# Kernel optimization log

Measured on AMD Instinct MI355X. Metric: run time of the kernel, lower is better.

The kernel has to match this reference:

```python
import jax, jax.numpy as jnp
import numpy as np

B, S, T = 64, 1024, 64
H, A, DA, DT, P, NT = 1024, 1024, 512, 256, 256, 32
DIN = DA + A + DT  # LSTMCell input: [a_tm1_embed, att_tm1, pre_type]


def setup_inputs() -> dict:
    key = jax.random.key(0)
    ks = jax.random.split(key, 16)
    nrm = lambda k, shape, s=0.02: jax.random.normal(k, shape, jnp.float32) * s
    return {
        'src_encodings': jax.random.normal(ks[0], (B, S, H), jnp.float32),
        'W_ih': nrm(ks[1], (4 * H, DIN)), 'b_ih': jnp.zeros((4 * H,), jnp.float32),
        'W_hh': nrm(ks[2], (4 * H, H)), 'b_hh': jnp.zeros((4 * H,), jnp.float32),
        'W_att': nrm(ks[3], (H, H)),            # att_sketch_linear (no bias)
        'W_attvec': nrm(ks[4], (A, 2 * H)),     # sketch_att_vec_linear (no bias)
        'W_init': nrm(ks[5], (H, H)), 'b_init': jnp.zeros((H,), jnp.float32),  # decoder_cell_init
        'W_q2a': nrm(ks[6], (DA, A)), 'b_q2a': jnp.zeros((DA,), jnp.float32),  # query_vec_to_action_embed
        'prod_embed': nrm(ks[7], (P, DA), 0.05), 'prod_bias': jnp.zeros((P,), jnp.float32),
        'type_embed': nrm(ks[8], (NT, DT), 0.05),
        'prev_prod_ids': jax.random.randint(ks[9], (B, T), 0, P),
        'prev_type_ids': jax.random.randint(ks[10], (B, T), 0, NT),
        'target_prod_ids': jax.random.randint(ks[11], (B, T), 0, P),
        'sketch_lens': jax.random.randint(ks[12], (B,), T // 2, T + 1),
        'src_lens': jax.random.randint(ks[13], (B,), S // 2, S + 1),
    }


def _lstm_cell(x, h, c, W_ih, b_ih, W_hh, b_hh):
    gates = x @ W_ih.T + b_ih + h @ W_hh.T + b_hh
    i, f, g, o = jnp.split(gates, 4, axis=-1)
    c_new = jax.nn.sigmoid(f) * c + jax.nn.sigmoid(i) * jnp.tanh(g)
    h_new = jax.nn.sigmoid(o) * jnp.tanh(c_new)
    return h_new, c_new


def reference(src_encodings, W_ih, b_ih, W_hh, b_hh, W_att, W_attvec, W_init, b_init,
              W_q2a, b_q2a, prod_embed, prod_bias, type_embed,
              prev_prod_ids, prev_type_ids, target_prod_ids, sketch_lens, src_lens):
    Bq, Sq, Hq = src_encodings.shape
    Tq = prev_prod_ids.shape[1]
    src_valid = jnp.arange(Sq)[None, :] < src_lens[:, None]            # [B,S] True = real token
    step_valid = jnp.arange(Tq)[None, :] < sketch_lens[:, None]        # [B,T]
    prev_valid = step_valid & (jnp.arange(Tq)[None, :] > 0)            # prev action exists

    src_att = jnp.einsum('bsh,kh->bsk', src_encodings, W_att)          # att_sketch_linear
    # init_decoder_state(adaptive_avg_pool1d(enc,1))
    init_cell = src_encodings.mean(axis=1)
    h0 = jnp.tanh(init_cell @ W_init.T + b_init)
    c0 = jnp.zeros_like(h0)
    att0 = jnp.zeros((Bq, A), src_encodings.dtype)

    # precomputed grammar lookups (production / type embeddings of a_{t-1})
    a_embeds = jnp.where(prev_valid[..., None], prod_embed[prev_prod_ids], 0.0)   # [B,T,DA]
    t_embeds = jnp.where(prev_valid[..., None], type_embed[prev_type_ids], 0.0)   # [B,T,DT]
    is_first = jnp.arange(Tq) == 0                                                # [T]

    def step(carry, inp):
        h, c, att_tm1 = carry
        a_e, t_e, first = inp
        x = jnp.concatenate([a_e, att_tm1, t_e], axis=-1)
        x = jnp.where(first, 0.0, x)                                   # t==0 -> zero input
        h, c = _lstm_cell(x, h, c, W_ih, b_ih, W_hh, b_hh)
        scores = jnp.einsum('bh,bsh->bs', h, src_att)
        scores = jnp.where(src_valid, scores, -1e9)
        alpha = jax.nn.softmax(scores, axis=-1)
        ctx = jnp.einsum('bs,bsh->bh', alpha, src_encodings)
        att_t = jnp.tanh(jnp.concatenate([h, ctx], axis=-1) @ W_attvec.T)
        q = jnp.tanh(att_t @ W_q2a.T + b_q2a)                          # non_linear readout
        probs = jax.nn.softmax(q @ prod_embed.T + prod_bias, axis=-1)  # [B,P]
        return (h, c, att_t), probs

    xs = (jnp.swapaxes(a_embeds, 0, 1), jnp.swapaxes(t_embeds, 0, 1), is_first)
    _, probs = jax.lax.scan(step, (h0, c0, att0), xs)                  # [T,B,P]

    tgt = jnp.swapaxes(target_prod_ids, 0, 1)[..., None]               # [T,B,1]
    p_t = jnp.take_along_axis(probs, tgt, axis=-1)[..., 0]             # [T,B]
    logp = jnp.log(p_t + 1e-8)
    sketch_prob = jnp.sum(jnp.where(step_valid.T, logp, 0.0), axis=0)  # [B]
    return sketch_prob
```

## Files before the change

kernel.cpp:

```cpp
#include <hip/hip_runtime.h>
#include <hip/hip_bf16.h>

typedef unsigned short u16;
typedef unsigned int u32;
typedef unsigned long long u64;
typedef __attribute__((ext_vector_type(8))) short short8;
typedef __attribute__((ext_vector_type(8))) u16 ushort8;
typedef __attribute__((ext_vector_type(4))) float f32x4;

__device__ __forceinline__ float bf2f(u16 x){ u32 u=((u32)x)<<16; return __builtin_bit_cast(float,u); }
__device__ __forceinline__ u16 f2bf(float f){ u32 u=__builtin_bit_cast(u32,f); u32 r=(u+0x7fffu+((u>>16)&1u))>>16; return (u16)r; }
__device__ __forceinline__ float sigf(float x){ return 1.f/(1.f+__expf(-x)); }

__device__ __forceinline__ void scf(float* p, float v){
  __hip_atomic_store(p, v, __ATOMIC_RELAXED, __HIP_MEMORY_SCOPE_AGENT);
}
__device__ __forceinline__ void scu16(u16* p, u16 v){
  __hip_atomic_store(p, v, __ATOMIC_RELAXED, __HIP_MEMORY_SCOPE_AGENT);
}


__global__ __launch_bounds__(256) void k_cast(const float* __restrict__ s, u16* __restrict__ d, long n){
  long i = ((long)blockIdx.x*256 + threadIdx.x)*8;
  if (i >= n) return;
  float4 a = *(const float4*)(s+i);
  float4 b = *(const float4*)(s+i+4);
  ushort8 o;
  o[0]=f2bf(a.x); o[1]=f2bf(a.y); o[2]=f2bf(a.z); o[3]=f2bf(a.w);
  o[4]=f2bf(b.x); o[5]=f2bf(b.y); o[6]=f2bf(b.z); o[7]=f2bf(b.w);
  *(ushort8*)(d+i) = o;
}

__global__ __launch_bounds__(256) void k_build_wc(const float* __restrict__ Wih, const float* __restrict__ Whh,
                                                  u16* __restrict__ WC){
  long i8 = (long)blockIdx.x*256 + threadIdx.x;
  if (i8 >= (long)4096*352) return;
  int j = (int)(i8/352); int kk = (int)(i8%352)*8;
  const float* src;
  if (kk < 512)        src = Wih + (long)j*1792 + kk;
  else if (kk < 768)   src = Wih + (long)j*1792 + (kk+1024);
  else if (kk < 1792)  src = Wih + (long)j*1792 + (kk-256);
  else                 src = Whh + (long)j*1024 + (kk-1792);
  u16* dst = WC + (long)j*2816 + kk;
  ushort8 o;
  #pragma unroll
  for (int q=0;q<8;++q) o[q] = f2bf(src[q]);
  *(ushort8*)dst = o;
}

__global__ __launch_bounds__(256) void k_wattT(const float* __restrict__ Wa, u16* __restrict__ WT){
  int id = blockIdx.x*256 + threadIdx.x;
  int m = id >> 10, k = id & 1023;
  WT[(long)m*1024 + k] = f2bf(Wa[(long)k*1024 + m]);
}

__global__ __launch_bounds__(256) void k_mean(const u16* __restrict__ ENC, u16* __restrict__ MEANB){
  int b = blockIdx.x, h = blockIdx.y*256 + threadIdx.x;
  const u16* p = ENC + ((long)b<<20) + h;
  float s = 0.f;
  for (int ss=0; ss<1024; ++ss) s += bf2f(p[(long)ss<<10]);
  MEANB[b*1024 + h] = f2bf(s * (1.f/1024.f));
}

__global__ __launch_bounds__(256) void k_embed(const float* __restrict__ pemb, const float* __restrict__ temb,
      const int* __restrict__ pid, const int* __restrict__ tid_, const int* __restrict__ slen,
      u16* __restrict__ XC){
  int t = blockIdx.x >> 6, b = blockIdx.x & 63;
  bool valid = (t>0) && (t < slen[b]);
  int pi = pid[b*64 + t], ti = tid_[b*64 + t];
  u16* dst = XC + (long)blockIdx.x*2816;
  for (int kk = threadIdx.x; kk < 768; kk += 256){
    float v = 0.f;
    if (valid) v = (kk<512) ? pemb[(long)pi*512 + kk] : temb[(long)ti*256 + (kk-512)];
    dst[kk] = f2bf(v);
  }
}

__global__ void k_assign(const int* __restrict__ slen, int* __restrict__ ASG){
  if (threadIdx.x != 0 || blockIdx.x != 0) return;
  int lenv[64]; long total = 0;
  for (int b=0;b<64;++b){ int L = slen[b]; if (L<1)L=1; if (L>1024)L=1024; lenv[b]=L; total+=L; }
  int cnt[64]; int sum=0;
  for (int b=0;b<64;++b){ int c = (int)(((long)256*lenv[b])/total); if (c<1)c=1; cnt[b]=c; sum+=c; }
  int rem = 256 - sum; int bi = 0;
  while (rem > 0){ cnt[bi&63]++; rem--; bi++; }
  while (rem < 0){ if (cnt[bi&63] > 1){ cnt[bi&63]--; rem++; } bi++; }
  int st = 0;
  for (int b=0;b<64;++b){
    ASG[1024+b] = cnt[b];
    ASG[1088+b] = st;
    for (int i=0;i<cnt[b];++i){ ASG[st+i] = b; ASG[256+st+i] = i; }
    st += cnt[b];
  }
}

template<int MODE>
__global__ __launch_bounds__(256) void k_gemm(const u16* __restrict__ A, long lda,
      const u16* __restrict__ W, int K, const float* __restrict__ bias,
      float* __restrict__ OF, long ldo, u16* __restrict__ OB1, long ldb1){
  int l = threadIdx.x & 63, w = threadIdx.x >> 6;
  int c = l & 15, g = l >> 4;
  int n0 = blockIdx.x*16, m0 = blockIdx.y*64;
  const u16* ap = A + (long)(m0 + w*16 + c)*lda + g*8;
  const u16* bp = W + (long)(n0 + c)*K + g*8;
  f32x4 acc = {0.f,0.f,0.f,0.f};
  int kit = K >> 5;
  #pragma unroll 4
  for (int kb=0; kb<kit; ++kb){
    short8 av = *(const short8*)(ap + kb*32);
    short8 bv = *(const short8*)(bp + kb*32);
    acc = __builtin_amdgcn_mfma_f32_16x16x32_bf16(av, bv, acc, 0, 0, 0);
  }
  #pragma unroll
  for (int r=0;r<4;++r){
    int row = m0 + w*16 + g*4 + r;
    int col = n0 + c;
    float v = acc[r];
    if (MODE==2){ OB1[(long)row*ldb1 + col] = f2bf(tanhf(v + bias[col])); }
    if (MODE==3){ OF[(long)row*ldo + col] = v + bias[col]; }
  }
}

__global__ __launch_bounds__(256) void k_loss(const float* __restrict__ LG, const int* __restrict__ tgt,
      const int* __restrict__ slen, float* __restrict__ out){
  int b = blockIdx.x;
  int w = threadIdx.x >> 6, l = threadIdx.x & 63;
  int len = slen[b];
  float accum = 0.f;
  for (int t = w; t < 64; t += 4){
    if (t >= len) continue;
    const float* lp = LG + ((long)(t*64 + b))*256;
    float v0=lp[l], v1=lp[l+64], v2=lp[l+128], v3=lp[l+192];
    float mx = fmaxf(fmaxf(v0,v1), fmaxf(v2,v3));
    #pragma unroll
    for (int off=32; off; off>>=1) mx = fmaxf(mx, __shfl_xor(mx, off));
    float s = __expf(v0-mx)+__expf(v1-mx)+__expf(v2-mx)+__expf(v3-mx);
    #pragma unroll
    for (int off=32; off; off>>=1) s += __shfl_xor(s, off);
    float ltg = lp[tgt[b*64 + t]];
    float p = __expf(ltg - mx)/s;
    accum += logf(p + 1e-8f);
  }
  __shared__ float sm[4];
  if (l == 0) sm[w] = accum;
  __syncthreads();
  if (threadIdx.x == 0) out[b] = sm[0]+sm[1]+sm[2]+sm[3];
}

__device__ __forceinline__ void gsync(int* __restrict__ bar, int& gen){
  gen += 1;
  __syncthreads();
  if (threadIdx.x == 0){
    int grp = blockIdx.x & 15;
    int prev = __hip_atomic_fetch_add(bar + grp*64, 1, __ATOMIC_RELAXED, __HIP_MEMORY_SCOPE_AGENT);
    if (prev == gen*16 - 1)
      __hip_atomic_fetch_add(bar + 1024, 1, __ATOMIC_RELAXED, __HIP_MEMORY_SCOPE_AGENT);
    while (__hip_atomic_load(bar + 1024, __ATOMIC_RELAXED, __HIP_MEMORY_SCOPE_AGENT) < gen*16)
      __builtin_amdgcn_s_sleep(1);
  }
  __syncthreads();
}

__global__ __launch_bounds__(1024,1) void k_decoder(
      const u16* __restrict__ ENC, const u16* __restrict__ WC,
      const u16* __restrict__ WAVT, const u16* __restrict__ WAVEC,
      const float* __restrict__ bih, const float* __restrict__ bhh,
      u16* __restrict__ XC, u16* __restrict__ ATT,
      float* __restrict__ HWT, float* __restrict__ PLT,
      u16* __restrict__ CTXBT, const int* __restrict__ src_lens,
      const int* __restrict__ ASG, int* __restrict__ BAR){
  const int tid = threadIdx.x;
  const int w = tid >> 6, l = tid & 63, c = l & 15, g = l >> 4;
  const int bx = blockIdx.x;
  int gen = 0;

  __shared__ float smem[12320];
  f32x4* lacc  = (f32x4*)smem;
  float* s_ctx = smem;
  float* s_ls  = smem + 12288;
  u16*   ldsc  = (u16*)smem;
  f32x4* lacc4 = (f32x4*)(smem + 8192);

  const int n0 = bx << 2;
  const int jrow = n0 + (c & 3) + ((c >> 2) << 10);
  const float biasj = bih[jrow] + bhh[jrow];
  const int kh = w >> 2, mt = w & 3;
  const int lbase = l & 0x33;
  float creg[4] = {0.f,0.f,0.f,0.f};
  const int mt2 = bx & 3, nt2 = bx >> 2;
  const int b3 = ASG[bx];
  const int ci3 = ASG[256 + bx];
  const int nch3 = ASG[1024 + b3];
  int len3 = src_lens[b3]; if (len3 < 1) len3 = 1; if (len3 > 1024) len3 = 1024;
  const int chunk3 = (len3 + nch3 - 1)/nch3;
  int s0 = ci3*chunk3;
  int s1 = s0 + chunk3; if (s1 > len3) s1 = len3; if (s0 > s1) s0 = s1;
  const int mt4 = bx & 3, nt4 = bx >> 2;
  const int b16 = tid >> 6, lane64 = tid & 63;

  for (int t = 0; t < 64; ++t){
    const u16* XCt = XC + (size_t)t*64*2816;
    u16* XCn = XC + (size_t)(t+1)*64*2816;
    const u16* Hcur = XCn + 1792;
    float* HW   = HWT  + ((size_t)t<<16);
    float* PL   = PLT  + ((size_t)t<<8);
    u16*  CTXB  = CTXBT + ((size_t)t<<18);

    {
      const u16* ap = XCt + (long)(mt*16 + c)*2816 + kh*704 + g*8;
      const u16* bp = WC  + (long)jrow*2816 + kh*704 + g*8;
      f32x4 acc = {0.f,0.f,0.f,0.f};
      #pragma unroll 11
      for (int kb=0; kb<22; ++kb){
        short8 av = *(const short8*)(ap + kb*32);
        short8 bv = *(const short8*)(bp + kb*32);
        acc = __builtin_amdgcn_mfma_f32_16x16x32_bf16(av, bv, acc, 0, 0, 0);
      }
      lacc[w*64 + l] = acc;
      __syncthreads();
      if (w < 4){
        f32x4 a0 = lacc[w*64 + l];
        f32x4 a1 = lacc[(w+4)*64 + l];
        f32x4 a2 = lacc[(w+8)*64 + l];
        f32x4 a3 = lacc[(w+12)*64 + l];
        #pragma unroll
        for (int r=0;r<4;++r){
          float val = a0[r] + a1[r] + a2[r] + a3[r] + biasj;
          float iv = __shfl(val, lbase);
          float fv = __shfl(val, lbase+4);
          float gv = __shfl(val, lbase+8);
          float ov = __shfl(val, lbase+12);
          if ((l & 12) == 0){
            float cn = sigf(fv)*creg[r] + sigf(iv)*tanhf(gv);
            float hn = sigf(ov)*tanhf(cn);
            creg[r] = cn;
            int b = w*16 + g*4 + r;
            int n = n0 + (l & 3);
            scu16(XCn + (long)b*2816 + 1792 + n, f2bf(hn));
          }
        }
      }
    }
    gsync(BAR, gen);

    {
      const u16* ap = Hcur + (long)(mt2*16 + c)*2816 + w*64 + g*8;
      const u16* bp = WAVT + (long)(nt2*16 + c)*1024 + w*64 + g*8;
      f32x4 acc = {0.f,0.f,0.f,0.f};
      #pragma unroll
      for (int kb=0; kb<2; ++kb){
        short8 av = *(const short8*)(ap + kb*32);
        short8 bv = *(const short8*)(bp + kb*32);
        acc = __builtin_amdgcn_mfma_f32_16x16x32_bf16(av, bv, acc, 0, 0, 0);
      }
      lacc[w*64 + l] = acc;
      __syncthreads();
      if (w == 0){
        f32x4 rd = lacc[l];
        #pragma unroll
        for (int w2=1; w2<16; ++w2) rd += lacc[w2*64 + l];
        #pragma unroll
        for (int r=0;r<4;++r)
          scf(HW + (long)(mt2*16 + g*4 + r)*1024 + nt2*16 + c, rd[r]);
      }
    }
    gsync(BAR, gen);

    {
      float hw[16], ctx[16];
      const float* hwp = HW + b3*1024 + l*16;
      #pragma unroll
      for (int jj=0;jj<4;++jj){
        float4 v = *(const float4*)(hwp + jj*4);
        hw[4*jj]=v.x; hw[4*jj+1]=v.y; hw[4*jj+2]=v.z; hw[4*jj+3]=v.w;
      }
      #pragma unroll
      for (int jj=0;jj<16;++jj) ctx[jj]=0.f;
      float lsum = 0.f;
      const u16* encb = ENC + (((long)b3)<<20);
      const int base = s0 + 2*w;
      uint4 pa0,pa1,pa2,pa3, pb0,pb1,pb2,pb3, pc0,pc1,pc2,pc3;
      {
        int rA0 = (base   < s1) ? base   : s0;
        int rA1 = (base+1 < s1) ? base+1 : s0;
        const u16* p0 = encb + ((long)rA0<<10) + l*16;
        const u16* p1 = encb + ((long)rA1<<10) + l*16;
        pa0=*(const uint4*)p0; pa1=*(const uint4*)(p0+8);
        pa2=*(const uint4*)p1; pa3=*(const uint4*)(p1+8);
        int sB = base+32;
        int rB0 = (sB   < s1) ? sB   : s0;
        int rB1 = (sB+1 < s1) ? sB+1 : s0;
        const u16* q0 = encb + ((long)rB0<<10) + l*16;
        const u16* q1 = encb + ((long)rB1<<10) + l*16;
        pb0=*(const uint4*)q0; pb1=*(const uint4*)(q0+8);
        pb2=*(const uint4*)q1; pb3=*(const uint4*)(q1+8);
      }
      for (int s = base; s < s1; s += 32){
        int sC = s + 64;
        int rC0 = (sC   < s1) ? sC   : s0;
        int rC1 = (sC+1 < s1) ? sC+1 : s0;
        const u16* r0p = encb + ((long)rC0<<10) + l*16;
        const u16* r1p = encb + ((long)rC1<<10) + l*16;
        pc0=*(const uint4*)r0p; pc1=*(const uint4*)(r0p+8);
        pc2=*(const uint4*)r1p; pc3=*(const uint4*)(r1p+8);
        float scA = 0.f, scB = 0.f;
        #pragma unroll
        for (int jj=0;jj<4;++jj){
          u32 xA0=((const u32*)&pa0)[jj], xA1=((const u32*)&pa1)[jj];
          u32 xB0=((const u32*)&pa2)[jj], xB1=((const u32*)&pa3)[jj];
          scA += bf2f((u16)(xA0&0xffff))*hw[2*jj]   + bf2f((u16)(xA0>>16))*hw[2*jj+1];
          scA += bf2f((u16)(xA1&0xffff))*hw[8+2*jj] + bf2f((u16)(xA1>>16))*hw[8+2*jj+1];
          scB += bf2f((u16)(xB0&0xffff))*hw[2*jj]   + bf2f((u16)(xB0>>16))*hw[2*jj+1];
          scB += bf2f((u16)(xB1&0xffff))*hw[8+2*jj] + bf2f((u16)(xB1>>16))*hw[8+2*jj+1];
        }
        #pragma unroll
        for (int off=32; off; off>>=1){
          scA += __shfl_xor(scA, off);
          scB += __shfl_xor(scB, off);
        }
        if (s+1 >= s1) scB = -1e30f;
        float peA = __expf(scA);
        float peB = __expf(scB);
        lsum += peA + peB;
        #pragma unroll
        for (int jj=0;jj<4;++jj){
          u32 xA0=((const u32*)&pa0)[jj], xA1=((const u32*)&pa1)[jj];
          u32 xB0=((const u32*)&pa2)[jj], xB1=((const u32*)&pa3)[jj];
          ctx[2*jj]     += peA*bf2f((u16)(xA0&0xffff)) + peB*bf2f((u16)(xB0&0xffff));
          ctx[2*jj+1]   += peA*bf2f((u16)(xA0>>16))    + peB*bf2f((u16)(xB0>>16));
          ctx[8+2*jj]   += peA*bf2f((u16)(xA1&0xffff)) + peB*bf2f((u16)(xB1&0xffff));
          ctx[8+2*jj+1] += peA*bf2f((u16)(xA1>>16))    + peB*bf2f((u16)(xB1>>16));
        }
        pa0=pb0; pa1=pb1; pa2=pb2; pa3=pb3;
        pb0=pc0; pb1=pc1; pb2=pc2; pb3=pc3;
      }
      if (l == 0) s_ls[w] = lsum;
      if (w < 8){
        #pragma unroll
        for (int jj=0;jj<16;++jj) s_ctx[w*1024 + l*16 + jj] = ctx[jj];
      }
      __syncthreads();
      if (w >= 8){
        #pragma unroll
        for (int jj=0;jj<16;++jj) s_ctx[(w-8)*1024 + l*16 + jj] += ctx[jj];
      }
      __syncthreads();
      {
        float v = 0.f;
        #pragma unroll
        for (int p=0;p<8;++p) v += s_ctx[p*1024 + tid];
        scu16(CTXB + (((long)bx)<<10) + tid, f2bf(v));
      }
      if (tid == 0){
        float L = 0.f;
        #pragma unroll
        for (int q=0;q<16;++q) L += s_ls[q];
        scf(PL + bx, L);
      }
    }
    gsync(BAR, gen);

    {
      int b = mt4*16 + b16;
      int st = ASG[1088 + b], nL = ASG[1024 + b];
      float L = 0.f;
      for (int p=0;p<nL;++p) L += PL[st+p];
      float inv = (L > 0.f) ? 1.f/L : 0.f;
      float acc16[16];
      #pragma unroll
      for (int q=0;q<16;++q) acc16[q] = 0.f;
      for (int p=0;p<nL;++p){
        const u16* row = CTXB + (((long)(st+p))<<10);
        #pragma unroll
        for (int q=0;q<2;++q){
          int mcol8 = (lane64 + q*64)*8;
          ushort8 v = *(const ushort8*)(row + mcol8);
          #pragma unroll
          for (int j=0;j<8;++j) acc16[q*8+j] += bf2f(v[j]);
        }
      }
      const int swz = (b16 & 7) << 3;
      #pragma unroll
      for (int q=0;q<2;++q){
        int mcol8 = (lane64 + q*64)*8;
        ushort8 o;
        #pragma unroll
        for (int j=0;j<8;++j) o[j] = f2bf(acc16[q*8+j]*inv);
        *(ushort8*)(ldsc + ((b16*1024 + mcol8) ^ swz)) = o;
      }
      __syncthreads();
      f32x4 acc = {0.f,0.f,0.f,0.f};
      const int koff = (w < 8) ? w*128 : 1024 + (w-8)*128;
      const u16* bp = WAVEC + (long)(nt4*16 + c)*2048 + koff + g*8;
      if (w < 8){
        const u16* ap = Hcur + (long)(mt4*16 + c)*2816 + w*128 + g*8;
        #pragma unroll
        for (int kb=0; kb<4; ++kb){
          short8 av = *(const short8*)(ap + kb*32);
          short8 bv = *(const short8*)(bp + kb*32);
          acc = __builtin_amdgcn_mfma_f32_16x16x32_bf16(av, bv, acc, 0, 0, 0);
        }
      } else {
        const int cswz = (c & 7) << 3;
        const int kbase = c*1024 + (w-8)*128 + g*8;
        #pragma unroll
        for (int kb=0; kb<4; ++kb){
          short8 av = *(const short8*)(ldsc + ((kbase + kb*32) ^ cswz));
          short8 bv = *(const short8*)(bp + kb*32);
          acc = __builtin_amdgcn_mfma_f32_16x16x32_bf16(av, bv, acc, 0, 0, 0);
        }
      }
      lacc4[w*64 + l] = acc;
      __syncthreads();
      if (w == 0){
        f32x4 rd = lacc4[l];
        #pragma unroll
        for (int w2=1; w2<16; ++w2) rd += lacc4[w2*64 + l];
        #pragma unroll
        for (int r=0;r<4;++r){
          int b_ = mt4*16 + g*4 + r;
          int col = nt4*16 + c;
          u16 x = f2bf(tanhf(rd[r]));
          scu16(XCn + (long)b_*2816 + 768 + col, x);
          ATT[((long)t*64 + b_)*1024 + col] = x;
        }
      }
    }
    gsync(BAR, gen);
  }
}

extern "C" void kernel_launch(void* const* d_in, const int* in_sizes, int n_in,
                              void* d_out, int out_size, void* d_ws, size_t ws_size,
                              hipStream_t stream){
  const float* enc      = (const float*)d_in[0];
  const float* W_ih     = (const float*)d_in[1];
  const float* b_ih     = (const float*)d_in[2];
  const float* W_hh     = (const float*)d_in[3];
  const float* b_hh     = (const float*)d_in[4];
  const float* W_att    = (const float*)d_in[5];
  const float* W_attvec = (const float*)d_in[6];
  const float* W_init   = (const float*)d_in[7];
  const float* b_init   = (const float*)d_in[8];
  const float* W_q2a    = (const float*)d_in[9];
  const float* b_q2a    = (const float*)d_in[10];
  const float* prod_emb = (const float*)d_in[11];
  const float* prod_bias= (const float*)d_in[12];
  const float* type_emb = (const float*)d_in[13];
  const int* prev_pid   = (const int*)d_in[14];
  const int* prev_tid   = (const int*)d_in[15];
  const int* target     = (const int*)d_in[16];
  const int* sk_lens    = (const int*)d_in[17];
  const int* src_lens   = (const int*)d_in[18];
  float* out = (float*)d_out;

  char* ws = (char*)d_ws;
  size_t o = 0;
  auto alloc = [&](size_t bytes)->char*{ char* p = ws + o; o += (bytes + 255) & ~(size_t)255; return p; };
  u16*  ENC  = (u16*)alloc((size_t)64*1024*1024*2);
  u16*  WC   = (u16*)alloc((size_t)4096*2816*2);
  u16*  WAVT = (u16*)alloc((size_t)1024*1024*2);
  u16*  WAVEC= (u16*)alloc((size_t)1024*2048*2);
  u16*  WQ   = (u16*)alloc((size_t)512*1024*2);
  u16*  PE   = (u16*)alloc((size_t)256*512*2);
  u16*  WINIT= (u16*)alloc((size_t)1024*1024*2);
  u16*  MEANB= (u16*)alloc((size_t)64*1024*2);
  u16*  XC   = (u16*)alloc((size_t)65*64*2816*2);
  u16*  ATT  = (u16*)alloc((size_t)64*64*1024*2);
  float* HWT = (float*)alloc((size_t)64*64*1024*4);
  float* PLT = (float*)alloc((size_t)64*256*4);
  u16*  CTXBT=(u16*)alloc((size_t)64*256*1024*2);
  u16*  Q    = (u16*)alloc((size_t)4096*512*2);
  float* LG  = (float*)alloc((size_t)4096*256*4);
  int*  BAR  = (int*)alloc(8192);
  int*  ASG  = (int*)alloc(8192);
  (void)ws_size; (void)in_sizes; (void)n_in; (void)out_size;

  hipMemsetAsync(XC, 0, (size_t)64*2816*2, stream);
  hipMemsetAsync(BAR, 0, 8192, stream);

  k_assign<<<1,64,0,stream>>>(src_lens, ASG);
  k_cast<<<32768,256,0,stream>>>(enc, ENC, (long)64*1024*1024);
  k_cast<<<1024,256,0,stream>>>(W_attvec, WAVEC, (long)1024*2048);
  k_cast<<<256,256,0,stream>>>(W_q2a, WQ, (long)512*1024);
  k_cast<<<64,256,0,stream>>>(prod_emb, PE, (long)256*512);
  k_cast<<<512,256,0,stream>>>(W_init, WINIT, (long)1024*1024);
  k_build_wc<<<5632,256,0,stream>>>(W_ih, W_hh, WC);
  k_wattT<<<4096,256,0,stream>>>(W_att, WAVT);
  k_mean<<<dim3(64,4),256,0,stream>>>(ENC, MEANB);
  k_gemm<2><<<dim3(64,1),256,0,stream>>>(MEANB, 1024L, WINIT, 1024, b_init,
                                         nullptr, 0L, XC + 1792, 2816L);
  k_embed<<<4096,256,0,stream>>>(prod_emb, type_emb, prev_pid, prev_tid, sk_lens, XC);

  k_decoder<<<256,1024,0,stream>>>(ENC, WC, WAVT, WAVEC, b_ih, b_hh,
                                   XC, ATT, HWT, PLT, CTXBT, src_lens, ASG, BAR);

  k_gemm<2><<<dim3(32,64),256,0,stream>>>(ATT, 1024L, WQ, 1024, b_q2a,
                                          nullptr, 0L, Q, 512L);
  k_gemm<3><<<dim3(16,64),256,0,stream>>>(Q, 512L, PE, 512, prod_bias,
                                          LG, 256L, nullptr, 0L);
  k_loss<<<64,256,0,stream>>>(LG, target, sk_lens, out);
}
```

Before: 4.395 ms.

## Precompute embedding gate contribution, relax barrier, prefetch encodings across steps

Moves the input-to-gate product for the action and type embeddings out of the recurrent loop into one batched GEMM before the decoder, so each step's LSTM matmul only covers attention and hidden inputs (K drops from 2816 to 2048). It replaces one global barrier with per-batch-group done counters, so blocks wait only for the context chunks their group needs. It also caps each batch at 8 chunks, which lets the chunk-sum reads be unrolled. Encoding rows are prefetched before the step loop and the reloads are moved after the attention loop, so the next step's loads overlap other work. The trade-offs are a 32MB buffer of precomputed gate values read every step and more complex synchronization.

```diff
diff --git a/kernel.cpp b/kernel.cpp
--- a/kernel.cpp
+++ b/kernel.cpp
@@ -64,11 +64,11 @@
 
 __global__ __launch_bounds__(256) void k_embed(const float* __restrict__ pemb, const float* __restrict__ temb,
       const int* __restrict__ pid, const int* __restrict__ tid_, const int* __restrict__ slen,
-      u16* __restrict__ XC){
+      u16* __restrict__ EMB){
   int t = blockIdx.x >> 6, b = blockIdx.x & 63;
   bool valid = (t>0) && (t < slen[b]);
   int pi = pid[b*64 + t], ti = tid_[b*64 + t];
-  u16* dst = XC + (long)blockIdx.x*2816;
+  u16* dst = EMB + (long)blockIdx.x*768;
   for (int kk = threadIdx.x; kk < 768; kk += 256){
     float v = 0.f;
     if (valid) v = (kk<512) ? pemb[(long)pi*512 + kk] : temb[(long)ti*256 + (kk-512)];
@@ -81,9 +81,12 @@
   int lenv[64]; long total = 0;
   for (int b=0;b<64;++b){ int L = slen[b]; if (L<1)L=1; if (L>1024)L=1024; lenv[b]=L; total+=L; }
   int cnt[64]; int sum=0;
-  for (int b=0;b<64;++b){ int c = (int)(((long)256*lenv[b])/total); if (c<1)c=1; cnt[b]=c; sum+=c; }
+  for (int b=0;b<64;++b){
+    int c = (int)(((long)256*lenv[b])/total);
+    if (c<1)c=1; if (c>8)c=8; cnt[b]=c; sum+=c;
+  }
   int rem = 256 - sum; int bi = 0;
-  while (rem > 0){ cnt[bi&63]++; rem--; bi++; }
+  while (rem > 0){ if (cnt[bi&63] < 8){ cnt[bi&63]++; rem--; } bi++; }
   while (rem < 0){ if (cnt[bi&63] > 1){ cnt[bi&63]--; rem++; } bi++; }
   int st = 0;
   for (int b=0;b<64;++b){
@@ -92,17 +95,22 @@
     for (int i=0;i<cnt[b];++i){ ASG[st+i] = b; ASG[256+st+i] = i; }
     st += cnt[b];
   }
+  for (int g=0; g<4; ++g){
+    int tg = 0;
+    for (int i=0;i<16;++i) tg += cnt[g*16+i];
+    ASG[1156+g] = tg;
+  }
 }
 
 template<int MODE>
 __global__ __launch_bounds__(256) void k_gemm(const u16* __restrict__ A, long lda,
-      const u16* __restrict__ W, int K, const float* __restrict__ bias,
+      const u16* __restrict__ W, long wld, int K, const float* __restrict__ bias,
       float* __restrict__ OF, long ldo, u16* __restrict__ OB1, long ldb1){
   int l = threadIdx.x & 63, w = threadIdx.x >> 6;
   int c = l & 15, g = l >> 4;
   int n0 = blockIdx.x*16, m0 = blockIdx.y*64;
   const u16* ap = A + (long)(m0 + w*16 + c)*lda + g*8;
-  const u16* bp = W + (long)(n0 + c)*K + g*8;
+  const u16* bp = W + (long)(n0 + c)*wld + g*8;
   f32x4 acc = {0.f,0.f,0.f,0.f};
   int kit = K >> 5;
   #pragma unroll 4
@@ -118,6 +126,7 @@
     float v = acc[r];
     if (MODE==2){ OB1[(long)row*ldb1 + col] = f2bf(tanhf(v + bias[col])); }
     if (MODE==3){ OF[(long)row*ldo + col] = v + bias[col]; }
+    if (MODE==4){ OB1[(long)row*ldb1 + col] = f2bf(v); }
   }
 }
 
@@ -164,11 +173,12 @@
 __global__ __launch_bounds__(1024,1) void k_decoder(
       const u16* __restrict__ ENC, const u16* __restrict__ WC,
       const u16* __restrict__ WAVT, const u16* __restrict__ WAVEC,
+      const u16* __restrict__ GEMB,
       const float* __restrict__ bih, const float* __restrict__ bhh,
       u16* __restrict__ XC, u16* __restrict__ ATT,
       float* __restrict__ HWT, float* __restrict__ PLT,
       u16* __restrict__ CTXBT, const int* __restrict__ src_lens,
-      const int* __restrict__ ASG, int* __restrict__ BAR){
+      const int* __restrict__ ASG, int* __restrict__ BAR, int* __restrict__ DONE){
   const int tid = threadIdx.x;
   const int w = tid >> 6, l = tid & 63, c = l & 15, g = l >> 4;
   const int bx = blockIdx.x;
@@ -191,27 +201,56 @@
   const int b3 = ASG[bx];
   const int ci3 = ASG[256 + bx];
   const int nch3 = ASG[1024 + b3];
+  const int g3 = b3 >> 4;
   int len3 = src_lens[b3]; if (len3 < 1) len3 = 1; if (len3 > 1024) len3 = 1024;
   const int chunk3 = (len3 + nch3 - 1)/nch3;
   int s0 = ci3*chunk3;
   int s1 = s0 + chunk3; if (s1 > len3) s1 = len3; if (s0 > s1) s0 = s1;
+  const u16* encb = ENC + (((long)b3)<<20);
+  const int base = s0 + 2*w;
   const int mt4 = bx & 3, nt4 = bx >> 2;
   const int b16 = tid >> 6, lane64 = tid & 63;
+  const int tgt4 = ASG[1156 + mt4];
+
+  uint4 pa0,pa1,pa2,pa3, pb0,pb1,pb2,pb3;
+  {
+    int rA0 = (base   < s1) ? base   : s0;
+    int rA1 = (base+1 < s1) ? base+1 : s0;
+    const u16* p0 = encb + ((long)rA0<<10) + l*16;
+    const u16* p1 = encb + ((long)rA1<<10) + l*16;
+    pa0=*(const uint4*)p0; pa1=*(const uint4*)(p0+8);
+    pa2=*(const uint4*)p1; pa3=*(const uint4*)(p1+8);
+    int sB = base+32;
+    int rB0 = (sB   < s1) ? sB   : s0;
+    int rB1 = (sB+1 < s1) ? sB+1 : s0;
+    const u16* q0 = encb + ((long)rB0<<10) + l*16;
+    const u16* q1 = encb + ((long)rB1<<10) + l*16;
+    pb0=*(const uint4*)q0; pb1=*(const uint4*)(q0+8);
+    pb2=*(const uint4*)q1; pb3=*(const uint4*)(q1+8);
+  }
 
   for (int t = 0; t < 64; ++t){
-    const u16* XCt = XC + (size_t)t*64*2816;
-    u16* XCn = XC + (size_t)(t+1)*64*2816;
-    const u16* Hcur = XCn + 1792;
+    const u16* XCt = XC + (size_t)t*64*2048;
+    u16* XCn = XC + (size_t)(t+1)*64*2048;
+    const u16* Hcur = XCn + 1024;
     float* HW   = HWT  + ((size_t)t<<16);
     float* PL   = PLT  + ((size_t)t<<8);
     u16*  CTXB  = CTXBT + ((size_t)t<<18);
 
     {
-      const u16* ap = XCt + (long)(mt*16 + c)*2816 + kh*704 + g*8;
-      const u16* bp = WC  + (long)jrow*2816 + kh*704 + g*8;
+      float gb[4];
+      if (w < 4){
+        #pragma unroll
+        for (int r=0;r<4;++r){
+          int b = w*16 + g*4 + r;
+          gb[r] = bf2f(GEMB[(((size_t)t*64 + b))*4096 + jrow]);
+        }
+      }
+      const u16* ap = XCt + (long)(mt*16 + c)*2048 + kh*512 + g*8;
+      const u16* bp = WC  + (long)jrow*2816 + 768 + kh*512 + g*8;
       f32x4 acc = {0.f,0.f,0.f,0.f};
-      #pragma unroll 11
-      for (int kb=0; kb<22; ++kb){
+      #pragma unroll 8
+      for (int kb=0; kb<16; ++kb){
         short8 av = *(const short8*)(ap + kb*32);
         short8 bv = *(const short8*)(bp + kb*32);
         acc = __builtin_amdgcn_mfma_f32_16x16x32_bf16(av, bv, acc, 0, 0, 0);
@@ -225,7 +264,7 @@
         f32x4 a3 = lacc[(w+12)*64 + l];
         #pragma unroll
         for (int r=0;r<4;++r){
-          float val = a0[r] + a1[r] + a2[r] + a3[r] + biasj;
+          float val = a0[r] + a1[r] + a2[r] + a3[r] + gb[r] + biasj;
           float iv = __shfl(val, lbase);
           float fv = __shfl(val, lbase+4);
           float gv = __shfl(val, lbase+8);
@@ -236,7 +275,7 @@
             creg[r] = cn;
             int b = w*16 + g*4 + r;
             int n = n0 + (l & 3);
-            scu16(XCn + (long)b*2816 + 1792 + n, f2bf(hn));
+            scu16(XCn + (long)b*2048 + 1024 + n, f2bf(hn));
           }
         }
       }
@@ -244,7 +283,7 @@
     gsync(BAR, gen);
 
     {
-      const u16* ap = Hcur + (long)(mt2*16 + c)*2816 + w*64 + g*8;
+      const u16* ap = Hcur + (long)(mt2*16 + c)*2048 + w*64 + g*8;
       const u16* bp = WAVT + (long)(nt2*16 + c)*1024 + w*64 + g*8;
       f32x4 acc = {0.f,0.f,0.f,0.f};
       #pragma unroll
@@ -277,9 +316,45 @@
       #pragma unroll
       for (int jj=0;jj<16;++jj) ctx[jj]=0.f;
       float lsum = 0.f;
-      const u16* encb = ENC + (((long)b3)<<20);
-      const int base = s0 + 2*w;
-      uint4 pa0,pa1,pa2,pa3, pb0,pb1,pb2,pb3, pc0,pc1,pc2,pc3;
+      for (int s = base; s < s1; s += 32){
+        int sC = s + 64;
+        int rC0 = (sC   < s1) ? sC   : s0;
+        int rC1 = (sC+1 < s1) ? sC+1 : s0;
+        const u16* r0p = encb + ((long)rC0<<10) + l*16;
+        const u16* r1p = encb + ((long)rC1<<10) + l*16;
+        uint4 pc0=*(const uint4*)r0p; uint4 pc1=*(const uint4*)(r0p+8);
+        uint4 pc2=*(const uint4*)r1p; uint4 pc3=*(const uint4*)(r1p+8);
+        float scA = 0.f, scB = 0.f;
+        #pragma unroll
+        for (int jj=0;jj<4;++jj){
+          u32 xA0=((const u32*)&pa0)[jj], xA1=((const u32*)&pa1)[jj];
+          u32 xB0=((const u32*)&pa2)[jj], xB1=((const u32*)&pa3)[jj];
+          scA += bf2f((u16)(xA0&0xffff))*hw[2*jj]   + bf2f((u16)(xA0>>16))*hw[2*jj+1];
+          scA += bf2f((u16)(xA1&0xffff))*hw[8+2*jj] + bf2f((u16)(xA1>>16))*hw[8+2*jj+1];
+          scB += bf2f((u16)(xB0&0xffff))*hw[2*jj]   + bf2f((u16)(xB0>>16))*hw[2*jj+1];
+          scB += bf2f((u16)(xB1&0xffff))*hw[8+2*jj] + bf2f((u16)(xB1>>16))*hw[8+2*jj+1];
+        }
+        #pragma unroll
+        for (int off=32; off; off>>=1){
+          scA += __shfl_xor(scA, off);
+          scB += __shfl_xor(scB, off);
+        }
+        if (s+1 >= s1) scB = -1e30f;
+        float peA = __expf(scA);
+        float peB = __expf(scB);
+        lsum += peA + peB;
+        #pragma unroll
+        for (int jj=0;jj<4;++jj){
+          u32 xA0=((const u32*)&pa0)[jj], xA1=((const u32*)&pa1)[jj];
+          u32 xB0=((const u32*)&pa2)[jj], xB1=((const u32*)&pa3)[jj];
+          ctx[2*jj]     += peA*bf2f((u16)(xA0&0xffff)) + peB*bf2f((u16)(xB0&0xffff));
+          ctx[2*jj+1]   += peA*bf2f((u16)(xA0>>16))    + peB*bf2f((u16)(xB0>>16));
+          ctx[8+2*jj]   += peA*bf2f((u16)(xA1&0xffff)) + peB*bf2f((u16)(xB1&0xffff));
+          ctx[8+2*jj+1] += peA*bf2f((u16)(xA1>>16))    + peB*bf2f((u16)(xB1>>16));
+        }
+        pa0=pb0; pa1=pb1; pa2=pb2; pa3=pb3;
+        pb0=pc0; pb1=pc1; pb2=pc2; pb3=pc3;
+      }
       {
         int rA0 = (base   < s1) ? base   : s0;
         int rA1 = (base+1 < s1) ? base+1 : s0;
@@ -295,45 +370,6 @@
         pb0=*(const uint4*)q0; pb1=*(const uint4*)(q0+8);
         pb2=*(const uint4*)q1; pb3=*(const uint4*)(q1+8);
       }
-      for (int s = base; s < s1; s += 32){
-        int sC = s + 64;
-        int rC0 = (sC   < s1) ? sC   : s0;
-        int rC1 = (sC+1 < s1) ? sC+1 : s0;
-        const u16* r0p = encb + ((long)rC0<<10) + l*16;
-        const u16* r1p = encb + ((long)rC1<<10) + l*16;
-        pc0=*(const uint4*)r0p; pc1=*(const uint4*)(r0p+8);
-        pc2=*(const uint4*)r1p; pc3=*(const uint4*)(r1p+8);
-        float scA = 0.f, scB = 0.f;
-        #pragma unroll
-        for (int jj=0;jj<4;++jj){
-          u32 xA0=((const u32*)&pa0)[jj], xA1=((const u32*)&pa1)[jj];
-          u32 xB0=((const u32*)&pa2)[jj], xB1=((const u32*)&pa3)[jj];
-          scA += bf2f((u16)(xA0&0xffff))*hw[2*jj]   + bf2f((u16)(xA0>>16))*hw[2*jj+1];
-          scA += bf2f((u16)(xA1&0xffff))*hw[8+2*jj] + bf2f((u16)(xA1>>16))*hw[8+2*jj+1];
-          scB += bf2f((u16)(xB0&0xffff))*hw[2*jj]   + bf2f((u16)(xB0>>16))*hw[2*jj+1];
-          scB += bf2f((u16)(xB1&0xffff))*hw[8+2*jj] + bf2f((u16)(xB1>>16))*hw[8+2*jj+1];
-        }
-        #pragma unroll
-        for (int off=32; off; off>>=1){
-          scA += __shfl_xor(scA, off);
-          scB += __shfl_xor(scB, off);
-        }
-        if (s+1 >= s1) scB = -1e30f;
-        float peA = __expf(scA);
-        float peB = __expf(scB);
-        lsum += peA + peB;
-        #pragma unroll
-        for (int jj=0;jj<4;++jj){
-          u32 xA0=((const u32*)&pa0)[jj], xA1=((const u32*)&pa1)[jj];
-          u32 xB0=((const u32*)&pa2)[jj], xB1=((const u32*)&pa3)[jj];
-          ctx[2*jj]     += peA*bf2f((u16)(xA0&0xffff)) + peB*bf2f((u16)(xB0&0xffff));
-          ctx[2*jj+1]   += peA*bf2f((u16)(xA0>>16))    + peB*bf2f((u16)(xB0>>16));
-          ctx[8+2*jj]   += peA*bf2f((u16)(xA1&0xffff)) + peB*bf2f((u16)(xB1&0xffff));
-          ctx[8+2*jj+1] += peA*bf2f((u16)(xA1>>16))    + peB*bf2f((u16)(xB1>>16));
-        }
-        pa0=pb0; pa1=pb1; pa2=pb2; pa3=pb3;
-        pb0=pc0; pb1=pc1; pb2=pc2; pb3=pc3;
-      }
       if (l == 0) s_ls[w] = lsum;
       if (w < 8){
         #pragma unroll
@@ -358,25 +394,47 @@
         scf(PL + bx, L);
       }
     }
-    gsync(BAR, gen);
+    __syncthreads();
+    if (tid == 0){
+      __hip_atomic_fetch_add(DONE + t*4 + g3, 1, __ATOMIC_RELAXED, __HIP_MEMORY_SCOPE_AGENT);
+      while (__hip_atomic_load(DONE + t*4 + mt4, __ATOMIC_RELAXED, __HIP_MEMORY_SCOPE_AGENT) < tgt4)
+        __builtin_amdgcn_s_sleep(1);
+    }
+    __syncthreads();
 
     {
       int b = mt4*16 + b16;
       int st = ASG[1088 + b], nL = ASG[1024 + b];
+      float plv[8];
+      #pragma unroll
+      for (int p=0;p<8;++p){ int ip = st + ((p<nL)? p:0); plv[p] = PL[ip]; }
       float L = 0.f;
-      for (int p=0;p<nL;++p) L += PL[st+p];
+      #pragma unroll
+      for (int p=0;p<8;++p) if (p<nL) L += plv[p];
       float inv = (L > 0.f) ? 1.f/L : 0.f;
       float acc16[16];
       #pragma unroll
       for (int q=0;q<16;++q) acc16[q] = 0.f;
-      for (int p=0;p<nL;++p){
-        const u16* row = CTXB + (((long)(st+p))<<10);
-        #pragma unroll
-        for (int q=0;q<2;++q){
-          int mcol8 = (lane64 + q*64)*8;
-          ushort8 v = *(const ushort8*)(row + mcol8);
-          #pragma unroll
-          for (int j=0;j<8;++j) acc16[q*8+j] += bf2f(v[j]);
+      #pragma unroll
+      for (int rnd=0; rnd<2; ++rnd){
+        ushort8 va[4][2];
+        #pragma unroll
+        for (int q4=0;q4<4;++q4){
+          int p = rnd*4+q4; int ip = st + ((p<nL)? p:0);
+          const u16* row = CTXB + (((long)ip)<<10);
+          va[q4][0] = *(const ushort8*)(row + lane64*8);
+          va[q4][1] = *(const ushort8*)(row + (lane64+64)*8);
+        }
+        #pragma unroll
+        for (int q4=0;q4<4;++q4){
+          int p = rnd*4+q4;
+          if (p<nL){
+            #pragma unroll
+            for (int j=0;j<8;++j){
+              acc16[j]   += bf2f(va[q4][0][j]);
+              acc16[8+j] += bf2f(va[q4][1][j]);
+            }
+          }
         }
       }
       const int swz = (b16 & 7) << 3;
@@ -393,7 +451,7 @@
       const int koff = (w < 8) ? w*128 : 1024 + (w-8)*128;
       const u16* bp = WAVEC + (long)(nt4*16 + c)*2048 + koff + g*8;
       if (w < 8){
-        const u16* ap = Hcur + (long)(mt4*16 + c)*2816 + w*128 + g*8;
+        const u16* ap = Hcur + (long)(mt4*16 + c)*2048 + w*128 + g*8;
         #pragma unroll
         for (int kb=0; kb<4; ++kb){
           short8 av = *(const short8*)(ap + kb*32);
@@ -421,7 +479,7 @@
           int b_ = mt4*16 + g*4 + r;
           int col = nt4*16 + c;
           u16 x = f2bf(tanhf(rd[r]));
-          scu16(XCn + (long)b_*2816 + 768 + col, x);
+          scu16(XCn + (long)b_*2048 + col, x);
           ATT[((long)t*64 + b_)*1024 + col] = x;
         }
       }
@@ -465,7 +523,9 @@
   u16*  PE   = (u16*)alloc((size_t)256*512*2);
   u16*  WINIT= (u16*)alloc((size_t)1024*1024*2);
   u16*  MEANB= (u16*)alloc((size_t)64*1024*2);
-  u16*  XC   = (u16*)alloc((size_t)65*64*2816*2);
+  u16*  EMB  = (u16*)alloc((size_t)4096*768*2);
+  u16*  GEMB = (u16*)alloc((size_t)4096*4096*2);
+  u16*  XC   = (u16*)alloc((size_t)65*64*2048*2);
   u16*  ATT  = (u16*)alloc((size_t)64*64*1024*2);
   float* HWT = (float*)alloc((size_t)64*64*1024*4);
   float* PLT = (float*)alloc((size_t)64*256*4);
@@ -473,11 +533,13 @@
   u16*  Q    = (u16*)alloc((size_t)4096*512*2);
   float* LG  = (float*)alloc((size_t)4096*256*4);
   int*  BAR  = (int*)alloc(8192);
+  int*  DONE = (int*)alloc(4096);
   int*  ASG  = (int*)alloc(8192);
   (void)ws_size; (void)in_sizes; (void)n_in; (void)out_size;
 
-  hipMemsetAsync(XC, 0, (size_t)64*2816*2, stream);
+  hipMemsetAsync(XC, 0, (size_t)64*2048*2, stream);
   hipMemsetAsync(BAR, 0, 8192, stream);
+  hipMemsetAsync(DONE, 0, 4096, stream);
 
   k_assign<<<1,64,0,stream>>>(src_lens, ASG);
   k_cast<<<32768,256,0,stream>>>(enc, ENC, (long)64*1024*1024);
@@ -488,16 +550,18 @@
   k_build_wc<<<5632,256,0,stream>>>(W_ih, W_hh, WC);
   k_wattT<<<4096,256,0,stream>>>(W_att, WAVT);
   k_mean<<<dim3(64,4),256,0,stream>>>(ENC, MEANB);
-  k_gemm<2><<<dim3(64,1),256,0,stream>>>(MEANB, 1024L, WINIT, 1024, b_init,
-                                         nullptr, 0L, XC + 1792, 2816L);
-  k_embed<<<4096,256,0,stream>>>(prod_emb, type_emb, prev_pid, prev_tid, sk_lens, XC);
-
-  k_decoder<<<256,1024,0,stream>>>(ENC, WC, WAVT, WAVEC, b_ih, b_hh,
-                                   XC, ATT, HWT, PLT, CTXBT, src_lens, ASG, BAR);
-
-  k_gemm<2><<<dim3(32,64),256,0,stream>>>(ATT, 1024L, WQ, 1024, b_q2a,
+  k_gemm<2><<<dim3(64,1),256,0,stream>>>(MEANB, 1024L, WINIT, 1024L, 1024, b_init,
+                                         nullptr, 0L, XC + 1024, 2048L);
+  k_embed<<<4096,256,0,stream>>>(prod_emb, type_emb, prev_pid, prev_tid, sk_lens, EMB);
+  k_gemm<4><<<dim3(256,64),256,0,stream>>>(EMB, 768L, WC, 2816L, 768, nullptr,
+                                           nullptr, 0L, GEMB, 4096L);
+
+  k_decoder<<<256,1024,0,stream>>>(ENC, WC, WAVT, WAVEC, GEMB, b_ih, b_hh,
+                                   XC, ATT, HWT, PLT, CTXBT, src_lens, ASG, BAR, DONE);
+
+  k_gemm<2><<<dim3(32,64),256,0,stream>>>(ATT, 1024L, WQ, 1024L, 1024, b_q2a,
                                           nullptr, 0L, Q, 512L);
-  k_gemm<3><<<dim3(16,64),256,0,stream>>>(Q, 512L, PE, 512, prod_bias,
+  k_gemm<3><<<dim3(16,64),256,0,stream>>>(Q, 512L, PE, 512L, 512, prod_bias,
                                           LG, 256L, nullptr, 0L);
   k_loss<<<64,256,0,stream>>>(LG, target, sk_lens, out);
 }
```

After: 5.857 ms. +33.3%, slower.

## Store encoder states as FP8 for decoder attention streaming

Applied to the files above, without the earlier changes.

Converts src_encodings to FP8 (e4m3 via cvt_pk_fp8) instead of bf16, halving the bytes streamed from HBM per decode step in the attention score/context loop. The mean for the initial cell state is now computed from the fp32 input directly. It also hoists the first prefetch before the time loop and re-issues it at the end of each step, caps per-batch chunk counts at 8, and unrolls the partial-context reduction with up-front loads. FP8 loses substantial precision in attention scores and context, which risks tolerance failures.

```diff
diff --git a/kernel.cpp b/kernel.cpp
--- a/kernel.cpp
+++ b/kernel.cpp
@@ -2,11 +2,13 @@
 #include <hip/hip_bf16.h>
 
 typedef unsigned short u16;
+typedef unsigned char u8;
 typedef unsigned int u32;
 typedef unsigned long long u64;
 typedef __attribute__((ext_vector_type(8))) short short8;
 typedef __attribute__((ext_vector_type(8))) u16 ushort8;
 typedef __attribute__((ext_vector_type(4))) float f32x4;
+typedef __attribute__((ext_vector_type(2))) float f32x2;
 
 __device__ __forceinline__ float bf2f(u16 x){ u32 u=((u32)x)<<16; return __builtin_bit_cast(float,u); }
 __device__ __forceinline__ u16 f2bf(float f){ u32 u=__builtin_bit_cast(u32,f); u32 r=(u+0x7fffu+((u>>16)&1u))>>16; return (u16)r; }
@@ -29,6 +31,20 @@
   o[0]=f2bf(a.x); o[1]=f2bf(a.y); o[2]=f2bf(a.z); o[3]=f2bf(a.w);
   o[4]=f2bf(b.x); o[5]=f2bf(b.y); o[6]=f2bf(b.z); o[7]=f2bf(b.w);
   *(ushort8*)(d+i) = o;
+}
+
+__global__ __launch_bounds__(256) void k_cast8(const float* __restrict__ s, u8* __restrict__ d, long n){
+  long i = ((long)blockIdx.x*256 + threadIdx.x)*8;
+  if (i >= n) return;
+  float4 a = *(const float4*)(s+i);
+  float4 b = *(const float4*)(s+i+4);
+  u32 w0 = 0, w1 = 0;
+  w0 = __builtin_amdgcn_cvt_pk_fp8_f32(a.x, a.y, w0, false);
+  w0 = __builtin_amdgcn_cvt_pk_fp8_f32(a.z, a.w, w0, true);
+  w1 = __builtin_amdgcn_cvt_pk_fp8_f32(b.x, b.y, w1, false);
+  w1 = __builtin_amdgcn_cvt_pk_fp8_f32(b.z, b.w, w1, true);
+  uint2 o; o.x = w0; o.y = w1;
+  *(uint2*)(d+i) = o;
 }
 
 __global__ __launch_bounds__(256) void k_build_wc(const float* __restrict__ Wih, const float* __restrict__ Whh,
@@ -54,11 +70,11 @@
   WT[(long)m*1024 + k] = f2bf(Wa[(long)k*1024 + m]);
 }
 
-__global__ __launch_bounds__(256) void k_mean(const u16* __restrict__ ENC, u16* __restrict__ MEANB){
+__global__ __launch_bounds__(256) void k_meanf(const float* __restrict__ enc, u16* __restrict__ MEANB){
   int b = blockIdx.x, h = blockIdx.y*256 + threadIdx.x;
-  const u16* p = ENC + ((long)b<<20) + h;
+  const float* p = enc + ((long)b<<20) + h;
   float s = 0.f;
-  for (int ss=0; ss<1024; ++ss) s += bf2f(p[(long)ss<<10]);
+  for (int ss=0; ss<1024; ++ss) s += p[(long)ss<<10];
   MEANB[b*1024 + h] = f2bf(s * (1.f/1024.f));
 }
 
@@ -81,9 +97,12 @@
   int lenv[64]; long total = 0;
   for (int b=0;b<64;++b){ int L = slen[b]; if (L<1)L=1; if (L>1024)L=1024; lenv[b]=L; total+=L; }
   int cnt[64]; int sum=0;
-  for (int b=0;b<64;++b){ int c = (int)(((long)256*lenv[b])/total); if (c<1)c=1; cnt[b]=c; sum+=c; }
+  for (int b=0;b<64;++b){
+    int c = (int)(((long)256*lenv[b])/total);
+    if (c<1)c=1; if (c>8)c=8; cnt[b]=c; sum+=c;
+  }
   int rem = 256 - sum; int bi = 0;
-  while (rem > 0){ cnt[bi&63]++; rem--; bi++; }
+  while (rem > 0){ if (cnt[bi&63] < 8){ cnt[bi&63]++; rem--; } bi++; }
   while (rem < 0){ if (cnt[bi&63] > 1){ cnt[bi&63]--; rem++; } bi++; }
   int st = 0;
   for (int b=0;b<64;++b){
@@ -162,7 +181,7 @@
 }
 
 __global__ __launch_bounds__(1024,1) void k_decoder(
-      const u16* __restrict__ ENC, const u16* __restrict__ WC,
+      const u8* __restrict__ ENC8, const u16* __restrict__ WC,
       const u16* __restrict__ WAVT, const u16* __restrict__ WAVEC,
       const float* __restrict__ bih, const float* __restrict__ bhh,
       u16* __restrict__ XC, u16* __restrict__ ATT,
@@ -195,8 +214,23 @@
   const int chunk3 = (len3 + nch3 - 1)/nch3;
   int s0 = ci3*chunk3;
   int s1 = s0 + chunk3; if (s1 > len3) s1 = len3; if (s0 > s1) s0 = s1;
+  const u8* encb = ENC8 + (((long)b3)<<20);
+  const int base = s0 + 2*w;
   const int mt4 = bx & 3, nt4 = bx >> 2;
   const int b16 = tid >> 6, lane64 = tid & 63;
+
+  uint4 pa0,pa1, pb0,pb1;
+  {
+    int rA0 = (base   < s1) ? base   : s0;
+    int rA1 = (base+1 < s1) ? base+1 : s0;
+    pa0 = *(const uint4*)(encb + ((long)rA0<<10) + l*16);
+    pa1 = *(const uint4*)(encb + ((long)rA1<<10) + l*16);
+    int sB = base+32;
+    int rB0 = (sB   < s1) ? sB   : s0;
+    int rB1 = (sB+1 < s1) ? sB+1 : s0;
+    pb0 = *(const uint4*)(encb + ((long)rB0<<10) + l*16);
+    pb1 = *(const uint4*)(encb + ((long)rB1<<10) + l*16);
+  }
 
   for (int t = 0; t < 64; ++t){
     const u16* XCt = XC + (size_t)t*64*2816;
@@ -277,42 +311,27 @@
       #pragma unroll
       for (int jj=0;jj<16;++jj) ctx[jj]=0.f;
       float lsum = 0.f;
-      const u16* encb = ENC + (((long)b3)<<20);
-      const int base = s0 + 2*w;
-      uint4 pa0,pa1,pa2,pa3, pb0,pb1,pb2,pb3, pc0,pc1,pc2,pc3;
-      {
-        int rA0 = (base   < s1) ? base   : s0;
-        int rA1 = (base+1 < s1) ? base+1 : s0;
-        const u16* p0 = encb + ((long)rA0<<10) + l*16;
-        const u16* p1 = encb + ((long)rA1<<10) + l*16;
-        pa0=*(const uint4*)p0; pa1=*(const uint4*)(p0+8);
-        pa2=*(const uint4*)p1; pa3=*(const uint4*)(p1+8);
-        int sB = base+32;
-        int rB0 = (sB   < s1) ? sB   : s0;
-        int rB1 = (sB+1 < s1) ? sB+1 : s0;
-        const u16* q0 = encb + ((long)rB0<<10) + l*16;
-        const u16* q1 = encb + ((long)rB1<<10) + l*16;
-        pb0=*(const uint4*)q0; pb1=*(const uint4*)(q0+8);
-        pb2=*(const uint4*)q1; pb3=*(const uint4*)(q1+8);
-      }
       for (int s = base; s < s1; s += 32){
         int sC = s + 64;
         int rC0 = (sC   < s1) ? sC   : s0;
         int rC1 = (sC+1 < s1) ? sC+1 : s0;
-        const u16* r0p = encb + ((long)rC0<<10) + l*16;
-        const u16* r1p = encb + ((long)rC1<<10) + l*16;
-        pc0=*(const uint4*)r0p; pc1=*(const uint4*)(r0p+8);
-        pc2=*(const uint4*)r1p; pc3=*(const uint4*)(r1p+8);
+        uint4 pc0 = *(const uint4*)(encb + ((long)rC0<<10) + l*16);
+        uint4 pc1 = *(const uint4*)(encb + ((long)rC1<<10) + l*16);
+        float eA[16], eB[16];
+        #pragma unroll
+        for (int jj=0;jj<4;++jj){
+          u32 xA = ((const u32*)&pa0)[jj];
+          u32 xB = ((const u32*)&pa1)[jj];
+          f32x2 la = __builtin_amdgcn_cvt_pk_f32_fp8(xA, false);
+          f32x2 ha = __builtin_amdgcn_cvt_pk_f32_fp8(xA, true);
+          f32x2 lb = __builtin_amdgcn_cvt_pk_f32_fp8(xB, false);
+          f32x2 hb = __builtin_amdgcn_cvt_pk_f32_fp8(xB, true);
+          eA[4*jj]=la[0]; eA[4*jj+1]=la[1]; eA[4*jj+2]=ha[0]; eA[4*jj+3]=ha[1];
+          eB[4*jj]=lb[0]; eB[4*jj+1]=lb[1]; eB[4*jj+2]=hb[0]; eB[4*jj+3]=hb[1];
+        }
         float scA = 0.f, scB = 0.f;
         #pragma unroll
-        for (int jj=0;jj<4;++jj){
-          u32 xA0=((const u32*)&pa0)[jj], xA1=((const u32*)&pa1)[jj];
-          u32 xB0=((const u32*)&pa2)[jj], xB1=((const u32*)&pa3)[jj];
-          scA += bf2f((u16)(xA0&0xffff))*hw[2*jj]   + bf2f((u16)(xA0>>16))*hw[2*jj+1];
-          scA += bf2f((u16)(xA1&0xffff))*hw[8+2*jj] + bf2f((u16)(xA1>>16))*hw[8+2*jj+1];
-          scB += bf2f((u16)(xB0&0xffff))*hw[2*jj]   + bf2f((u16)(xB0>>16))*hw[2*jj+1];
-          scB += bf2f((u16)(xB1&0xffff))*hw[8+2*jj] + bf2f((u16)(xB1>>16))*hw[8+2*jj+1];
-        }
+        for (int jj=0;jj<16;++jj){ scA += eA[jj]*hw[jj]; scB += eB[jj]*hw[jj]; }
         #pragma unroll
         for (int off=32; off; off>>=1){
           scA += __shfl_xor(scA, off);
@@ -323,16 +342,20 @@
         float peB = __expf(scB);
         lsum += peA + peB;
         #pragma unroll
-        for (int jj=0;jj<4;++jj){
-          u32 xA0=((const u32*)&pa0)[jj], xA1=((const u32*)&pa1)[jj];
-          u32 xB0=((const u32*)&pa2)[jj], xB1=((const u32*)&pa3)[jj];
-          ctx[2*jj]     += peA*bf2f((u16)(xA0&0xffff)) + peB*bf2f((u16)(xB0&0xffff));
-          ctx[2*jj+1]   += peA*bf2f((u16)(xA0>>16))    + peB*bf2f((u16)(xB0>>16));
-          ctx[8+2*jj]   += peA*bf2f((u16)(xA1&0xffff)) + peB*bf2f((u16)(xB1&0xffff));
-          ctx[8+2*jj+1] += peA*bf2f((u16)(xA1>>16))    + peB*bf2f((u16)(xB1>>16));
-        }
-        pa0=pb0; pa1=pb1; pa2=pb2; pa3=pb3;
-        pb0=pc0; pb1=pc1; pb2=pc2; pb3=pc3;
+        for (int jj=0;jj<16;++jj) ctx[jj] += peA*eA[jj] + peB*eB[jj];
+        pa0=pb0; pa1=pb1;
+        pb0=pc0; pb1=pc1;
+      }
+      {
+        int rA0 = (base   < s1) ? base   : s0;
+        int rA1 = (base+1 < s1) ? base+1 : s0;
+        pa0 = *(const uint4*)(encb + ((long)rA0<<10) + l*16);
+        pa1 = *(const uint4*)(encb + ((long)rA1<<10) + l*16);
+        int sB = base+32;
+        int rB0 = (sB   < s1) ? sB   : s0;
+        int rB1 = (sB+1 < s1) ? sB+1 : s0;
+        pb0 = *(const uint4*)(encb + ((long)rB0<<10) + l*16);
+        pb1 = *(const uint4*)(encb + ((long)rB1<<10) + l*16);
       }
       if (l == 0) s_ls[w] = lsum;
       if (w < 8){
@@ -363,20 +386,36 @@
     {
       int b = mt4*16 + b16;
       int st = ASG[1088 + b], nL = ASG[1024 + b];
+      float plv[8];
+      #pragma unroll
+      for (int p=0;p<8;++p){ int ip = st + ((p<nL)? p:0); plv[p] = PL[ip]; }
       float L = 0.f;
-      for (int p=0;p<nL;++p) L += PL[st+p];
+      #pragma unroll
+      for (int p=0;p<8;++p) if (p<nL) L += plv[p];
       float inv = (L > 0.f) ? 1.f/L : 0.f;
       float acc16[16];
       #pragma unroll
       for (int q=0;q<16;++q) acc16[q] = 0.f;
-      for (int p=0;p<nL;++p){
-        const u16* row = CTXB + (((long)(st+p))<<10);
-        #pragma unroll
-        for (int q=0;q<2;++q){
-          int mcol8 = (lane64 + q*64)*8;
-          ushort8 v = *(const ushort8*)(row + mcol8);
-          #pragma unroll
-          for (int j=0;j<8;++j) acc16[q*8+j] += bf2f(v[j]);
+      #pragma unroll
+      for (int rnd=0; rnd<2; ++rnd){
+        ushort8 va[4][2];
+        #pragma unroll
+        for (int q4=0;q4<4;++q4){
+          int p = rnd*4+q4; int ip = st + ((p<nL)? p:0);
+          const u16* row = CTXB + (((long)ip)<<10);
+          va[q4][0] = *(const ushort8*)(row + lane64*8);
+          va[q4][1] = *(const ushort8*)(row + (lane64+64)*8);
+        }
+        #pragma unroll
+        for (int q4=0;q4<4;++q4){
+          int p = rnd*4+q4;
+          if (p<nL){
+            #pragma unroll
+            for (int j=0;j<8;++j){
+              acc16[j]   += bf2f(va[q4][0][j]);
+              acc16[8+j] += bf2f(va[q4][1][j]);
+            }
+          }
         }
       }
       const int swz = (b16 & 7) << 3;
@@ -457,7 +496,7 @@
   char* ws = (char*)d_ws;
   size_t o = 0;
   auto alloc = [&](size_t bytes)->char*{ char* p = ws + o; o += (bytes + 255) & ~(size_t)255; return p; };
-  u16*  ENC  = (u16*)alloc((size_t)64*1024*1024*2);
+  u8*   ENC8 = (u8*)alloc((size_t)64*1024*1024);
   u16*  WC   = (u16*)alloc((size_t)4096*2816*2);
   u16*  WAVT = (u16*)alloc((size_t)1024*1024*2);
   u16*  WAVEC= (u16*)alloc((size_t)1024*2048*2);
@@ -480,19 +519,19 @@
   hipMemsetAsync(BAR, 0, 8192, stream);
 
   k_assign<<<1,64,0,stream>>>(src_lens, ASG);
-  k_cast<<<32768,256,0,stream>>>(enc, ENC, (long)64*1024*1024);
+  k_cast8<<<32768,256,0,stream>>>(enc, ENC8, (long)64*1024*1024);
   k_cast<<<1024,256,0,stream>>>(W_attvec, WAVEC, (long)1024*2048);
   k_cast<<<256,256,0,stream>>>(W_q2a, WQ, (long)512*1024);
   k_cast<<<64,256,0,stream>>>(prod_emb, PE, (long)256*512);
   k_cast<<<512,256,0,stream>>>(W_init, WINIT, (long)1024*1024);
   k_build_wc<<<5632,256,0,stream>>>(W_ih, W_hh, WC);
   k_wattT<<<4096,256,0,stream>>>(W_att, WAVT);
-  k_mean<<<dim3(64,4),256,0,stream>>>(ENC, MEANB);
+  k_meanf<<<dim3(64,4),256,0,stream>>>(enc, MEANB);
   k_gemm<2><<<dim3(64,1),256,0,stream>>>(MEANB, 1024L, WINIT, 1024, b_init,
                                          nullptr, 0L, XC + 1792, 2816L);
   k_embed<<<4096,256,0,stream>>>(prod_emb, type_emb, prev_pid, prev_tid, sk_lens, XC);
 
-  k_decoder<<<256,1024,0,stream>>>(ENC, WC, WAVT, WAVEC, b_ih, b_hh,
+  k_decoder<<<256,1024,0,stream>>>(ENC8, WC, WAVT, WAVEC, b_ih, b_hh,
                                    XC, ATT, HWT, PLT, CTXBT, src_lens, ASG, BAR);
 
   k_gemm<2><<<dim3(32,64),256,0,stream>>>(ATT, 1024L, WQ, 1024, b_q2a,
```

Measured after the change: 4.290 ms. 2.4% less time.
